# Kernel optimization log

Hardware: AMD Instinct MI355X
Metric: run time of the kernel (lower is better)

The kernel has to match this reference:

```python
import jax, jax.numpy as jnp
import numpy as np

DIM = 1024
NUM_HEADS = 16
DIM_HEAD = 64
POOL = 8  # int(sqrt(agent_num=64))
SCALE = DIM_HEAD ** -0.5


def setup_inputs() -> dict:
    key = jax.random.key(0)
    k1, k2, k3, k4 = jax.random.split(key, 4)
    inner = NUM_HEADS * DIM_HEAD
    x = jax.random.normal(k1, (4, 4096, DIM), dtype=jnp.float32)
    # qkv Linear (no bias): weight stored as (in, out) so forward is x @ Wqkv
    Wqkv = jax.random.normal(k2, (DIM, 3 * inner), dtype=jnp.float32) * (DIM ** -0.5)
    Wo = jax.random.normal(k3, (inner, DIM), dtype=jnp.float32) * (inner ** -0.5)
    bo = jax.random.normal(k4, (DIM,), dtype=jnp.float32) * 0.01
    return {"x": x, "Wqkv": Wqkv, "Wo": Wo, "bo": bo}


def reference(x, Wqkv, Wo, bo):
    b, t, _ = x.shape
    h, d = NUM_HEADS, DIM_HEAD
    qkv = x @ Wqkv                                   # [b, t, 3*h*d]
    qkv = qkv.reshape(b, t, 3, h, d)                 # split (qkv h d)
    qkv = jnp.transpose(qkv, (2, 0, 3, 1, 4))        # [3, b, h, t, d]
    q, k, v = qkv[0], qkv[1], qkv[2]
    # AdaptiveAvgPool2d((POOL, d)) on [b,h,t,d]: identity on d, mean-pool t -> POOL
    # (t divisible by POOL -> exact reshape+mean)
    agent = q.reshape(b, h, POOL, t // POOL, d).mean(axis=3)  # [b, h, P, d]
    # stage 1: agents attend over keys, aggregate values
    s1 = jnp.einsum('bhid,bhjd->bhij', agent * SCALE, k)      # [b, h, P, t]
    p1 = jax.nn.softmax(s1, axis=-1)
    v_agent = jnp.einsum('bhij,bhjd->bhid', p1, v)            # [b, h, P, d]
    # stage 2: queries attend over agent tokens
    s2 = jnp.einsum('bhid,bhjd->bhij', q * SCALE, agent)      # [b, h, t, P]
    p2 = jax.nn.softmax(s2, axis=-1)
    out = jnp.einsum('bhij,bhjd->bhid', p2, v_agent)          # [b, h, t, d]
    out = jnp.transpose(out, (0, 2, 1, 3)).reshape(b, t, h * d)
    return out @ Wo + bo
```

## Files before the change

### kernel.cpp

```cpp
#include <hip/hip_runtime.h>
#include <hip/hip_bf16.h>
#include <stdint.h>

typedef __bf16 bf16;
typedef __attribute__((ext_vector_type(8))) __bf16 bf16x8;
typedef __attribute__((ext_vector_type(4))) float f32x4;
typedef __attribute__((ext_vector_type(4))) unsigned int u32x4;

#define NH 16
#define DH 64
#define POOL 8
#define BATCH 4
#define SEQ 4096
#define DIMV 1024
#define QKV_N (3*DIMV)
#define M_TOTAL (BATCH*SEQ)
#define SCALE_F 0.125f
#define AGS_F (SCALE_F / 512.0f)
#define BH (BATCH*NH)
#define QKVSZ ((size_t)BH*SEQ*DH)
#define TCH 16
#define TCL (SEQ/TCH)
#define HP 128

#define AS1(p) ((const __attribute__((address_space(1))) void*)(p))
#define AS3(p) ((__attribute__((address_space(3))) void*)(p))
typedef const __attribute__((address_space(3))) char* lds_cp;

__global__ void prep(const float* __restrict__ x, bf16* __restrict__ xb,
                     const float* __restrict__ Wqkv, bf16* __restrict__ WqkvT,
                     const float* __restrict__ Wo, bf16* __restrict__ WoT) {
  __shared__ float tile[32][33];
  const int b = blockIdx.x;
  if (b < 8192) {
    size_t i = ((size_t)b * 256 + threadIdx.x) * 8;
    float4 f0 = *(const float4*)(x + i);
    float4 f1 = *(const float4*)(x + i + 4);
    bf16x8 o;
    o[0] = (bf16)f0.x; o[1] = (bf16)f0.y; o[2] = (bf16)f0.z; o[3] = (bf16)f0.w;
    o[4] = (bf16)f1.x; o[5] = (bf16)f1.y; o[6] = (bf16)f1.z; o[7] = (bf16)f1.w;
    *(bf16x8*)(xb + i) = o;
    return;
  }
  const float* in; bf16* out; int C, bx, by;
  if (b < 8192 + 3072) { int bb = b - 8192;  in = Wqkv; out = WqkvT; C = QKV_N; bx = bb % 96; by = bb / 96; }
  else                 { int bb = b - 11264; in = Wo;   out = WoT;   C = DIMV;  bx = bb % 32; by = bb / 32; }
  const int R = DIMV;
  int c0 = bx * 32, r0 = by * 32;
  int tx = threadIdx.x & 31, ty = threadIdx.x >> 5;
  for (int i = ty; i < 32; i += 8)
    tile[i][tx] = in[(size_t)(r0 + i) * C + c0 + tx];
  __syncthreads();
  for (int i = ty; i < 32; i += 8)
    out[(size_t)(c0 + i) * R + r0 + tx] = (bf16)tile[tx][i];
}

__global__ __launch_bounds__(512, 2)
void gemm1_qkv(const bf16* __restrict__ A, const bf16* __restrict__ B,
               bf16* __restrict__ qkvOut, float* __restrict__ agentSum) {
  constexpr int K1 = DIMV;
  constexpr int NI = K1 / 128;

  __shared__ __align__(16) bf16 LA[2][2][8192];
  __shared__ __align__(16) bf16 LB[2][2][8192];

  const int tid  = threadIdx.x;
  const int w    = tid >> 6;
  const int lane = tid & 63;
  const int wm = (w >> 2) * 128;
  const int wn = (w & 3) * 64;

  const int bid = blockIdx.x;
  const int swz = (bid & 7) * 96 + (bid >> 3);
  const int m0 = (swz / 12) * 256;
  const int n0 = (swz % 12) * 256;

  const int rT  = tid >> 3;
  const int csT = (((tid & 7) ^ (rT & 7)) << 3);
  const bf16* Ag = A + (size_t)(m0 + rT) * K1 + csT;
  const bf16* Bg = B + (size_t)(n0 + rT) * K1 + csT;

  const int rA = lane & 15, C = lane >> 4, xr = rA & 7;
  const unsigned s0 = (unsigned)(((0 * 4 + C) ^ xr) << 4);
  const unsigned s1 = (unsigned)(((1 * 4 + C) ^ xr) << 4);
  const unsigned aoff = (unsigned)((wm + rA) << 7);
  const unsigned boff = (unsigned)((wn + rA) << 7);

  f32x4 acc[8][4] = {};
  u32x4 aR[4][2], bR[4][2];

#define STG(arr, Gp, half, kofs) do {                                         \
    const bf16* _s = (Gp) + (size_t)((half) * 128) * K1 + (kofs);             \
    char* _d = (char*)&arr[half][0] + (w << 10);                              \
    __builtin_amdgcn_global_load_lds(AS1(_s), AS3(_d), 16, 0, 0);             \
    __builtin_amdgcn_global_load_lds(AS1(_s + 64 * K1), AS3(_d + 8192), 16, 0, 0); \
  } while (0)

#define DSR0(d, p)    asm volatile("ds_read_b128 %0, %1" : "=v"(d) : "v"(p))
#define DSR(d, p, o)  asm volatile("ds_read_b128 %0, %1 offset:" o : "=v"(d) : "v"(p))

#define READS_A(LAb, qm) do {                                                 \
    lds_cp _p0 = (lds_cp)(const char*)&LAb[0][0] + aoff + s0 + (qm) * 8192;   \
    lds_cp _p1 = (lds_cp)(const char*)&LAb[0][0] + aoff + s1 + (qm) * 8192;   \
    DSR0(aR[0][0], _p0); DSR(aR[1][0], _p0, "2048");                          \
    DSR(aR[2][0], _p0, "4096"); DSR(aR[3][0], _p0, "6144");                   \
    DSR0(aR[0][1], _p1); DSR(aR[1][1], _p1, "2048");                          \
    DSR(aR[2][1], _p1, "4096"); DSR(aR[3][1], _p1, "6144");                   \
  } while (0)

#define READS_B01(LBb) do {                                                   \
    lds_cp _p0 = (lds_cp)(const char*)&LBb[0][0] + boff + s0;                 \
    lds_cp _p1 = (lds_cp)(const char*)&LBb[0][0] + boff + s1;                 \
    DSR0(bR[0][0], _p0); DSR(bR[1][0], _p0, "2048");                          \
    DSR0(bR[0][1], _p1); DSR(bR[1][1], _p1, "2048");                          \
  } while (0)

#define READS_B23(LBb) do {                                                   \
    lds_cp _p0 = (lds_cp)(const char*)&LBb[0][0] + boff + s0;                 \
    lds_cp _p1 = (lds_cp)(const char*)&LBb[0][0] + boff + s1;                 \
    DSR(bR[2][0], _p0, "4096"); DSR(bR[3][0], _p0, "6144");                   \
    DSR(bR[2][1], _p1, "4096"); DSR(bR[3][1], _p1, "6144");                   \
  } while (0)

#define WAITL8 do { asm volatile("s_waitcnt lgkmcnt(8)");                     \
                    __builtin_amdgcn_sched_barrier(0); } while (0)

#define MFMA_Q(qm, qn) do {                                                   \
    asm volatile("s_waitcnt lgkmcnt(0)");                                     \
    __builtin_amdgcn_sched_barrier(0);                                        \
    __builtin_amdgcn_s_setprio(1);                                            \
    _Pragma("unroll")                                                         \
    for (int il = 0; il < 4; ++il)                                            \
      _Pragma("unroll")                                                       \
      for (int jj = 0; jj < 2; ++jj) {                                        \
        f32x4& ac = acc[(qm) * 4 + il][(qn) * 2 + jj];                        \
        ac = __builtin_amdgcn_mfma_f32_16x16x32_bf16(                         \
            __builtin_bit_cast(bf16x8, aR[il][0]),                            \
            __builtin_bit_cast(bf16x8, bR[(qn) * 2 + jj][0]), ac, 0, 0, 0);   \
        ac = __builtin_amdgcn_mfma_f32_16x16x32_bf16(                         \
            __builtin_bit_cast(bf16x8, aR[il][1]),                            \
            __builtin_bit_cast(bf16x8, bR[(qn) * 2 + jj][1]), ac, 0, 0, 0);   \
      }                                                                       \
    __builtin_amdgcn_s_setprio(0);                                            \
    __builtin_amdgcn_sched_barrier(0);                                        \
  } while (0)

#define BAR __builtin_amdgcn_s_barrier()

  STG(LA[0], Ag, 0, 0); STG(LA[0], Ag, 1, 0);
  STG(LB[0], Bg, 0, 0); STG(LB[0], Bg, 1, 0);
  STG(LB[1], Bg, 0, 64); STG(LB[1], Bg, 1, 64);
  asm volatile("s_waitcnt vmcnt(4)");
  __builtin_amdgcn_sched_barrier(0);
  BAR;

  int kk = 0;
  for (int i = 0; i < NI - 1; ++i, kk += 128) {
    READS_A(LA[0], 0); READS_B01(LB[0]);
    STG(LA[1], Ag, 0, kk + 64);
    WAITL8;
    BAR; MFMA_Q(0, 0); BAR;
    READS_B23(LB[0]);
    STG(LA[1], Ag, 1, kk + 64);
    BAR; MFMA_Q(0, 1); BAR;
    READS_A(LA[0], 1);
    STG(LB[0], Bg, 0, kk + 128);
    BAR; MFMA_Q(1, 0); BAR;
    STG(LB[0], Bg, 1, kk + 128);
    BAR; MFMA_Q(1, 1);
    asm volatile("s_waitcnt vmcnt(4)");
    __builtin_amdgcn_sched_barrier(0);
    BAR;
    READS_A(LA[1], 0); READS_B01(LB[1]);
    STG(LA[0], Ag, 0, kk + 128);
    WAITL8;
    BAR; MFMA_Q(0, 0); BAR;
    READS_B23(LB[1]);
    STG(LA[0], Ag, 1, kk + 128);
    BAR; MFMA_Q(0, 1); BAR;
    READS_A(LA[1], 1);
    STG(LB[1], Bg, 0, kk + 192);
    BAR; MFMA_Q(1, 0); BAR;
    STG(LB[1], Bg, 1, kk + 192);
    BAR; MFMA_Q(1, 1);
    asm volatile("s_waitcnt vmcnt(4)");
    __builtin_amdgcn_sched_barrier(0);
    BAR;
  }
  READS_A(LA[0], 0); READS_B01(LB[0]);
  STG(LA[1], Ag, 0, kk + 64);
  WAITL8;
  BAR; MFMA_Q(0, 0); BAR;
  READS_B23(LB[0]);
  STG(LA[1], Ag, 1, kk + 64);
  BAR; MFMA_Q(0, 1); BAR;
  READS_A(LA[0], 1);
  BAR; MFMA_Q(1, 0); BAR;
  MFMA_Q(1, 1);
  asm volatile("s_waitcnt vmcnt(0)");
  __builtin_amdgcn_sched_barrier(0);
  BAR;
  READS_A(LA[1], 0); READS_B01(LB[1]);
  WAITL8;
  BAR; MFMA_Q(0, 0); BAR;
  READS_B23(LB[1]);
  BAR; MFMA_Q(0, 1); BAR;
  READS_A(LA[1], 1);
  BAR; MFMA_Q(1, 0); BAR;
  MFMA_Q(1, 1);

#undef STG
#undef DSR0
#undef DSR
#undef READS_A
#undef READS_B01
#undef READS_B23
#undef WAITL8
#undef MFMA_Q
#undef BAR

  const int cr = (lane >> 4) * 4;
  const int cc = lane & 15;
  const int ncol  = n0 + wn;
  const int which = ncol >> 10;
  const int hh    = (ncol >> 6) & 15;
  const int rowb  = m0 + wm;
  const int bb_   = rowb >> 12;
  const int tb    = rowb & 4095;
  bf16* Cp = qkvOut + (size_t)which * QKVSZ + (size_t)(bb_ * NH + hh) * SEQ * DH;
#pragma unroll
  for (int i = 0; i < 8; ++i)
#pragma unroll
    for (int j = 0; j < 4; ++j)
#pragma unroll
      for (int r = 0; r < 4; ++r)
        Cp[(size_t)(tb + i * 16 + cr + r) * DH + j * 16 + cc] = (bf16)acc[i][j][r];

  if (which == 0) {
    const int pp = tb >> 9;
    float* ag = agentSum + ((size_t)(bb_ * NH + hh) * POOL + pp) * DH;
#pragma unroll
    for (int j = 0; j < 4; ++j) {
      float s = 0.f;
#pragma unroll
      for (int i = 0; i < 8; ++i)
        s += acc[i][j][0] + acc[i][j][1] + acc[i][j][2] + acc[i][j][3];
      s += __shfl_xor(s, 16);
      s += __shfl_xor(s, 32);
      if (lane < 16) atomicAdd(&ag[j * 16 + lane], s);
    }
  }
}

__global__ __launch_bounds__(512, 2)
void gemm2_256(const bf16* __restrict__ A, const bf16* __restrict__ B,
               float* __restrict__ Out, const float* __restrict__ bias) {
  constexpr int K2 = HP;

  __shared__ __align__(16) bf16 LA[2][2][8192];
  __shared__ __align__(16) bf16 LB[2][2][8192];

  const int tid  = threadIdx.x;
  const int w    = tid >> 6;
  const int lane = tid & 63;
  const int wm = (w >> 2) * 128;
  const int wn = (w & 3) * 64;

  const int bid = blockIdx.x;
  const int swz = (bid & 7) * 32 + (bid >> 3);
  const int m0 = (swz >> 2) * 256;
  const int n0 = (swz & 3) * 256;

  const int rT  = tid >> 3;
  const int csT = (((tid & 7) ^ (rT & 7)) << 3);
  const bf16* Ag = A + (size_t)(m0 + rT) * K2 + csT;
  const bf16* Bg = B + ((size_t)(m0 >> 12) * DIMV + n0 + rT) * K2 + csT;

  const int rA = lane & 15, C = lane >> 4, xr = rA & 7;
  const unsigned s0 = (unsigned)(((0 * 4 + C) ^ xr) << 4);
  const unsigned s1 = (unsigned)(((1 * 4 + C) ^ xr) << 4);
  const unsigned aoff = (unsigned)((wm + rA) << 7);
  const unsigned boff = (unsigned)((wn + rA) << 7);

  f32x4 acc[8][4] = {};
  u32x4 aR[4][2], bR[4][2];

#define STG(arr, Gp, half, kofs) do {                                         \
    const bf16* _s = (Gp) + (size_t)((half) * 128) * K2 + (kofs);             \
    char* _d = (char*)&arr[half][0] + (w << 10);                              \
    __builtin_amdgcn_global_load_lds(AS1(_s), AS3(_d), 16, 0, 0);             \
    __builtin_amdgcn_global_load_lds(AS1(_s + 64 * K2), AS3(_d + 8192), 16, 0, 0); \
  } while (0)

#define DSR0(d, p)    asm volatile("ds_read_b128 %0, %1" : "=v"(d) : "v"(p))
#define DSR(d, p, o)  asm volatile("ds_read_b128 %0, %1 offset:" o : "=v"(d) : "v"(p))

#define READS_A(LAb, qm) do {                                                 \
    lds_cp _p0 = (lds_cp)(const char*)&LAb[0][0] + aoff + s0 + (qm) * 8192;   \
    lds_cp _p1 = (lds_cp)(const char*)&LAb[0][0] + aoff + s1 + (qm) * 8192;   \
    DSR0(aR[0][0], _p0); DSR(aR[1][0], _p0, "2048");                          \
    DSR(aR[2][0], _p0, "4096"); DSR(aR[3][0], _p0, "6144");                   \
    DSR0(aR[0][1], _p1); DSR(aR[1][1], _p1, "2048");                          \
    DSR(aR[2][1], _p1, "4096"); DSR(aR[3][1], _p1, "6144");                   \
  } while (0)

#define READS_B01(LBb) do {                                                   \
    lds_cp _p0 = (lds_cp)(const char*)&LBb[0][0] + boff + s0;                 \
    lds_cp _p1 = (lds_cp)(const char*)&LBb[0][0] + boff + s1;                 \
    DSR0(bR[0][0], _p0); DSR(bR[1][0], _p0, "2048");                          \
    DSR0(bR[0][1], _p1); DSR(bR[1][1], _p1, "2048");                          \
  } while (0)

#define READS_B23(LBb) do {                                                   \
    lds_cp _p0 = (lds_cp)(const char*)&LBb[0][0] + boff + s0;                 \
    lds_cp _p1 = (lds_cp)(const char*)&LBb[0][0] + boff + s1;                 \
    DSR(bR[2][0], _p0, "4096"); DSR(bR[3][0], _p0, "6144");                   \
    DSR(bR[2][1], _p1, "4096"); DSR(bR[3][1], _p1, "6144");                   \
  } while (0)

#define WAITL8 do { asm volatile("s_waitcnt lgkmcnt(8)");                     \
                    __builtin_amdgcn_sched_barrier(0); } while (0)

#define MFMA_Q(qm, qn) do {                                                   \
    asm volatile("s_waitcnt lgkmcnt(0)");                                     \
    __builtin_amdgcn_sched_barrier(0);                                        \
    __builtin_amdgcn_s_setprio(1);                                            \
    _Pragma("unroll")                                                         \
    for (int il = 0; il < 4; ++il)                                            \
      _Pragma("unroll")                                                       \
      for (int jj = 0; jj < 2; ++jj) {                                        \
        f32x4& ac = acc[(qm) * 4 + il][(qn) * 2 + jj];                        \
        ac = __builtin_amdgcn_mfma_f32_16x16x32_bf16(                         \
            __builtin_bit_cast(bf16x8, aR[il][0]),                            \
            __builtin_bit_cast(bf16x8, bR[(qn) * 2 + jj][0]), ac, 0, 0, 0);   \
        ac = __builtin_amdgcn_mfma_f32_16x16x32_bf16(                         \
            __builtin_bit_cast(bf16x8, aR[il][1]),                            \
            __builtin_bit_cast(bf16x8, bR[(qn) * 2 + jj][1]), ac, 0, 0, 0);   \
      }                                                                       \
    __builtin_amdgcn_s_setprio(0);                                            \
    __builtin_amdgcn_sched_barrier(0);                                        \
  } while (0)

#define BAR __builtin_amdgcn_s_barrier()

  STG(LA[0], Ag, 0, 0); STG(LA[0], Ag, 1, 0);
  STG(LB[0], Bg, 0, 0); STG(LB[0], Bg, 1, 0);
  STG(LB[1], Bg, 0, 64); STG(LB[1], Bg, 1, 64);
  asm volatile("s_waitcnt vmcnt(4)");
  __builtin_amdgcn_sched_barrier(0);
  BAR;

  READS_A(LA[0], 0); READS_B01(LB[0]);
  STG(LA[1], Ag, 0, 64);
  WAITL8;
  BAR; MFMA_Q(0, 0); BAR;
  READS_B23(LB[0]);
  STG(LA[1], Ag, 1, 64);
  BAR; MFMA_Q(0, 1); BAR;
  READS_A(LA[0], 1);
  BAR; MFMA_Q(1, 0); BAR;
  MFMA_Q(1, 1);
  asm volatile("s_waitcnt vmcnt(0)");
  __builtin_amdgcn_sched_barrier(0);
  BAR;
  READS_A(LA[1], 0); READS_B01(LB[1]);
  WAITL8;
  BAR; MFMA_Q(0, 0); BAR;
  READS_B23(LB[1]);
  BAR; MFMA_Q(0, 1); BAR;
  READS_A(LA[1], 1);
  BAR; MFMA_Q(1, 0); BAR;
  MFMA_Q(1, 1);

#undef STG
#undef DSR0
#undef DSR
#undef READS_A
#undef READS_B01
#undef READS_B23
#undef WAITL8
#undef MFMA_Q
#undef BAR

  const int cr = (lane >> 4) * 4;
  const int cc = lane & 15;
  const int rowb = m0 + wm;
  float bb4[4];
#pragma unroll
  for (int j = 0; j < 4; ++j) bb4[j] = bias[n0 + wn + j * 16 + cc];
#pragma unroll
  for (int i = 0; i < 8; ++i)
#pragma unroll
    for (int j = 0; j < 4; ++j) {
      const int col = n0 + wn + j * 16 + cc;
#pragma unroll
      for (int r = 0; r < 4; ++r)
        Out[(size_t)(rowb + i * 16 + cr + r) * DIMV + col] = acc[i][j][r] + bb4[j];
    }
}

__global__ __launch_bounds__(256)
void attn_mid(const bf16* __restrict__ q, const bf16* __restrict__ k,
              const bf16* __restrict__ v, const float* __restrict__ agentSum,
              bf16* __restrict__ P2,
              float* __restrict__ pm, float* __restrict__ pl,
              float* __restrict__ pva) {
  const int tc = blockIdx.x, bh = blockIdx.y;
  const int tid = threadIdx.x;
  const int t0 = tc * TCL;

  __shared__ float agT[64][8];
  __shared__ float se[TCL][9];
  __shared__ float rm[4][8], rl[4][8];

  for (int i = tid; i < 512; i += 256) {
    int p = i >> 6, d = i & 63;
    agT[d][p] = agentSum[(size_t)bh * 512 + i] * AGS_F;
  }
  __syncthreads();

  const bf16* qrow = q + ((size_t)bh * SEQ + t0 + tid) * DH;
  const bf16* krow = k + ((size_t)bh * SEQ + t0 + tid) * DH;
  bf16x8 qv8[8], kv8[8];
#pragma unroll
  for (int dc = 0; dc < 8; ++dc) {
    qv8[dc] = *(const bf16x8*)(qrow + dc * 8);
    kv8[dc] = *(const bf16x8*)(krow + dc * 8);
  }
  float scq[8] = {}, sck[8] = {};
#pragma unroll
  for (int dc = 0; dc < 8; ++dc) {
#pragma unroll
    for (int e = 0; e < 8; ++e) {
      float qv = (float)qv8[dc][e];
      float kv = (float)kv8[dc][e];
      int d = dc * 8 + e;
      float4 a0 = *(const float4*)&agT[d][0];
      float4 a1 = *(const float4*)&agT[d][4];
      scq[0] += a0.x * qv; scq[1] += a0.y * qv; scq[2] += a0.z * qv; scq[3] += a0.w * qv;
      scq[4] += a1.x * qv; scq[5] += a1.y * qv; scq[6] += a1.z * qv; scq[7] += a1.w * qv;
      sck[0] += a0.x * kv; sck[1] += a0.y * kv; sck[2] += a0.z * kv; sck[3] += a0.w * kv;
      sck[4] += a1.x * kv; sck[5] += a1.y * kv; sck[6] += a1.z * kv; sck[7] += a1.w * kv;
    }
  }

  {
    float m = scq[0];
#pragma unroll
    for (int p = 1; p < 8; ++p) m = fmaxf(m, scq[p]);
    float wsum = 0.f, wgt[8];
#pragma unroll
    for (int p = 0; p < 8; ++p) { wgt[p] = __expf(scq[p] - m); wsum += wgt[p]; }
    float inv = 1.0f / wsum;
    int b = bh >> 4, h = bh & 15;
    bf16x8 o8;
#pragma unroll
    for (int p = 0; p < 8; ++p) o8[p] = (bf16)(wgt[p] * inv);
    *(bf16x8*)&P2[((size_t)(b * SEQ + t0 + tid)) * HP + h * 8] = o8;
  }

  float mx[8];
#pragma unroll
  for (int p = 0; p < 8; ++p) mx[p] = sck[p];
#pragma unroll
  for (int o = 32; o; o >>= 1)
#pragma unroll
    for (int p = 0; p < 8; ++p) mx[p] = fmaxf(mx[p], __shfl_xor(mx[p], o));
  if ((tid & 63) == 0)
#pragma unroll
    for (int p = 0; p < 8; ++p) rm[tid >> 6][p] = mx[p];
  __syncthreads();
  float m[8];
#pragma unroll
  for (int p = 0; p < 8; ++p)
    m[p] = fmaxf(fmaxf(rm[0][p], rm[1][p]), fmaxf(rm[2][p], rm[3][p]));

  float sl[8];
#pragma unroll
  for (int p = 0; p < 8; ++p) {
    float e = __expf(sck[p] - m[p]);
    se[tid][p] = e;
    sl[p] = e;
  }
#pragma unroll
  for (int o = 32; o; o >>= 1)
#pragma unroll
    for (int p = 0; p < 8; ++p) sl[p] += __shfl_xor(sl[p], o);
  if ((tid & 63) == 0)
#pragma unroll
    for (int p = 0; p < 8; ++p) rl[tid >> 6][p] = sl[p];
  __syncthreads();
  if (tid < 8) {
    float l = rl[0][tid] + rl[1][tid] + rl[2][tid] + rl[3][tid];
    pm[(size_t)(bh * TCH + tc) * 8 + tid] = m[tid];
    pl[(size_t)(bh * TCH + tc) * 8 + tid] = l;
  }
  __syncthreads();

  const int lane = tid & 63;
  const int wv = tid >> 6;
  const int dg = lane & 7;
  const int to = lane >> 3;
  const int p0 = wv * 2;
  const bf16* vb = v + ((size_t)bh * SEQ + t0 + to) * DH + dg * 8;
  float a0[8] = {}, a1[8] = {};
  for (int tl = to; tl < TCL; tl += 8) {
    bf16x8 v8 = *(const bf16x8*)(vb + (size_t)(tl - to) * DH);
    float w0 = se[tl][p0];
    float w1 = se[tl][p0 + 1];
#pragma unroll
    for (int e = 0; e < 8; ++e) {
      float vf = (float)v8[e];
      a0[e] += w0 * vf;
      a1[e] += w1 * vf;
    }
  }
#pragma unroll
  for (int o = 8; o <= 32; o <<= 1) {
#pragma unroll
    for (int e = 0; e < 8; ++e) {
      a0[e] += __shfl_xor(a0[e], o);
      a1[e] += __shfl_xor(a1[e], o);
    }
  }
  if (to == 0) {
    float* o0 = pva + ((size_t)(bh * TCH + tc) * 8 + p0) * DH + dg * 8;
    float* o1 = o0 + DH;
#pragma unroll
    for (int e = 0; e < 8; ++e) { o0[e] = a0[e]; o1[e] = a1[e]; }
  }
}

__global__ void combine_vag(const float* __restrict__ pm, const float* __restrict__ pl,
                            const float* __restrict__ pva, float* __restrict__ vag) {
  int bh = blockIdx.x;
#pragma unroll
  for (int e = threadIdx.x; e < 512; e += 256) {
    int p = e >> 6, d = e & 63;
    float M = -1e30f;
#pragma unroll
    for (int tc = 0; tc < TCH; ++tc)
      M = fmaxf(M, pm[(size_t)(bh * TCH + tc) * 8 + p]);
    float L = 0.f, acc = 0.f;
#pragma unroll
    for (int tc = 0; tc < TCH; ++tc) {
      float w = __expf(pm[(size_t)(bh * TCH + tc) * 8 + p] - M);
      L   += w * pl[(size_t)(bh * TCH + tc) * 8 + p];
      acc += w * pva[((size_t)(bh * TCH + tc) * 8 + p) * DH + d];
    }
    vag[(size_t)bh * 512 + e] = acc / L;
  }
}

__global__ void w2_build(const float* __restrict__ vag, const bf16* __restrict__ WoT,
                         bf16* __restrict__ W2T) {
  int b = blockIdx.y;
  int n = blockIdx.x * 16 + (threadIdx.x & 15);
  int h = threadIdx.x >> 4;
  __shared__ float vg[128][65];
  for (int i = threadIdx.x; i < 128 * 64; i += 256)
    vg[i >> 6][i & 63] = vag[(size_t)b * 128 * 64 + i];
  __syncthreads();
  float acc[8] = {};
  const bf16* wrow = WoT + (size_t)n * DIMV + h * 64;
#pragma unroll
  for (int dv = 0; dv < 8; ++dv) {
    bf16x8 wv = *(const bf16x8*)(wrow + dv * 8);
#pragma unroll
    for (int e = 0; e < 8; ++e) {
      float wf = (float)wv[e];
      int d = dv * 8 + e;
#pragma unroll
      for (int p = 0; p < 8; ++p) acc[p] += vg[h * 8 + p][d] * wf;
    }
  }
  bf16x8 o;
#pragma unroll
  for (int p = 0; p < 8; ++p) o[p] = (bf16)acc[p];
  *(bf16x8*)&W2T[((size_t)b * DIMV + n) * HP + h * 8] = o;
}

extern "C" void kernel_launch(void* const* d_in, const int* in_sizes, int n_in,
                              void* d_out, int out_size, void* d_ws, size_t ws_size,
                              hipStream_t stream) {
  const float* x    = (const float*)d_in[0];
  const float* Wqkv = (const float*)d_in[1];
  const float* Wo   = (const float*)d_in[2];
  const float* bo   = (const float*)d_in[3];
  float* out = (float*)d_out;

  char* ws = (char*)d_ws;
  bf16* WqkvT = (bf16*)ws;                                   ws += (size_t)QKV_N * DIMV * 2;
  bf16* WoT   = (bf16*)ws;                                   ws += (size_t)DIMV * DIMV * 2;
  bf16* qkv   = (bf16*)ws;                                   ws += 3 * QKVSZ * 2;
  char* wsu   = ws;                                          ws += (size_t)M_TOTAL * DIMV * 2;
  bf16*  xb    = (bf16*)wsu;
  bf16*  P2    = (bf16*)wsu;
  bf16*  W2T   = (bf16*)(wsu + (size_t)M_TOTAL * HP * 2);
  float* agent = (float*)ws;                                 ws += 512 * 64 * 4;
  float* pm    = (float*)ws;                                 ws += BH * TCH * 8 * 4;
  float* pl    = (float*)ws;                                 ws += BH * TCH * 8 * 4;
  float* pva   = (float*)ws;                                 ws += (size_t)BH * TCH * 8 * DH * 4;
  float* vag   = (float*)ws;                                 ws += 512 * 64 * 4;

  const bf16* qp = qkv;
  const bf16* kp = qkv + QKVSZ;
  const bf16* vp = qkv + 2 * QKVSZ;

  hipMemsetAsync(agent, 0, 512 * 64 * 4, stream);

  prep<<<12288, 256, 0, stream>>>(x, xb, Wqkv, WqkvT, Wo, WoT);

  gemm1_qkv<<<768, 512, 0, stream>>>(xb, WqkvT, qkv, agent);

  attn_mid<<<dim3(TCH, BH), 256, 0, stream>>>(qp, kp, vp, agent, P2, pm, pl, pva);

  combine_vag<<<BH, 256, 0, stream>>>(pm, pl, pva, vag);
  w2_build<<<dim3(DIMV / 16, BATCH), 256, 0, stream>>>(vag, WoT, W2T);

  gemm2_256<<<256, 512, 0, stream>>>(P2, W2T, out, bo);
}
```

Before: 295.3 us.

## Fold agent projection into weights; skip materializing Q and K

```diff
diff --git a/kernel.cpp b/kernel.cpp
--- a/kernel.cpp
+++ b/kernel.cpp
@@ -18,7 +18,6 @@
 #define SCALE_F 0.125f
 #define AGS_F (SCALE_F / 512.0f)
 #define BH (BATCH*NH)
-#define QKVSZ ((size_t)BH*SEQ*DH)
 #define TCH 16
 #define TCL (SEQ/TCH)
 #define HP 128
@@ -43,8 +42,8 @@
     return;
   }
   const float* in; bf16* out; int C, bx, by;
-  if (b < 8192 + 3072) { int bb = b - 8192;  in = Wqkv; out = WqkvT; C = QKV_N; bx = bb % 96; by = bb / 96; }
-  else                 { int bb = b - 11264; in = Wo;   out = WoT;   C = DIMV;  bx = bb % 32; by = bb / 32; }
+  if (b < 9216) { int bb = b - 8192; in = Wqkv; out = WqkvT; C = QKV_N; bx = 64 + (bb & 31); by = bb >> 5; }
+  else          { int bb = b - 9216; in = Wo;   out = WoT;   C = DIMV;  bx = bb & 31;        by = bb >> 5; }
   const int R = DIMV;
   int c0 = bx * 32, r0 = by * 32;
   int tx = threadIdx.x & 31, ty = threadIdx.x >> 5;
@@ -55,9 +54,75 @@
     out[(size_t)(c0 + i) * R + r0 + tx] = (bf16)tile[tx][i];
 }
 
+__global__ void pool_x(const bf16* __restrict__ xb, float* __restrict__ xpool) {
+  const int bid = blockIdx.x;
+  const int bucket = bid >> 3, slice = bid & 7;
+  const int b = bucket >> 3, p = bucket & 7;
+  const int tid = threadIdx.x;
+  const int co = tid & 127;
+  const int r0 = tid >> 7;
+  const bf16* src = xb + ((size_t)b * SEQ + p * 512 + slice * 64 + r0) * DIMV + co * 8;
+  float a[8] = {};
+  for (int r = 0; r < 64; r += 2) {
+    bf16x8 v = *(const bf16x8*)(src + (size_t)r * DIMV);
+#pragma unroll
+    for (int e = 0; e < 8; ++e) a[e] += (float)v[e];
+  }
+  float* dst = xpool + (size_t)bucket * DIMV + co * 8;
+#pragma unroll
+  for (int e = 0; e < 8; ++e) atomicAdd(&dst[e], a[e]);
+}
+
+__global__ void agent_build(const float* __restrict__ xpool, const float* __restrict__ Wqkv,
+                            float* __restrict__ agent_s) {
+  __shared__ float xp[256];
+  const int bid = blockIdx.x;
+  const int bp = bid >> 2, cs = bid & 3;
+  const int tid = threadIdx.x;
+  xp[tid] = xpool[(size_t)bp * DIMV + cs * 256 + tid];
+  __syncthreads();
+  float acc[4] = {};
+  const float* wbase = Wqkv + (size_t)(cs * 256) * QKV_N + tid * 4;
+#pragma unroll 8
+  for (int c = 0; c < 256; ++c) {
+    float xv = xp[c];
+    float4 wv = *(const float4*)(wbase + (size_t)c * QKV_N);
+    acc[0] += xv * wv.x; acc[1] += xv * wv.y; acc[2] += xv * wv.z; acc[3] += xv * wv.w;
+  }
+  float* dst = agent_s + (size_t)bp * DIMV + tid * 4;
+#pragma unroll
+  for (int j = 0; j < 4; ++j) atomicAdd(&dst[j], acc[j]);
+}
+
+__global__ void w2cat_build(const float* __restrict__ agent_s, const float* __restrict__ Wqkv,
+                            bf16* __restrict__ scw) {
+  __shared__ float ag[8][64];
+  const int bid = blockIdx.x;
+  const int ct = bid & 3, qk = (bid >> 2) & 1, h = (bid >> 3) & 15, b = bid >> 7;
+  const int tid = threadIdx.x;
+  for (int i = tid; i < 512; i += 256)
+    ag[i >> 6][i & 63] = agent_s[(size_t)(b * 8 + (i >> 6)) * DIMV + h * 64 + (i & 63)];
+  __syncthreads();
+  const int c = ct * 256 + tid;
+  const float* wrow = Wqkv + (size_t)c * QKV_N + qk * 1024 + h * 64;
+  float wv[64];
+#pragma unroll
+  for (int d4 = 0; d4 < 16; ++d4) {
+    float4 w4 = *(const float4*)(wrow + d4 * 4);
+    wv[d4 * 4] = w4.x; wv[d4 * 4 + 1] = w4.y; wv[d4 * 4 + 2] = w4.z; wv[d4 * 4 + 3] = w4.w;
+  }
+#pragma unroll
+  for (int p = 0; p < 8; ++p) {
+    float s = 0.f;
+#pragma unroll
+    for (int d = 0; d < 64; ++d) s += wv[d] * ag[p][d];
+    scw[((size_t)b * 256 + qk * 128 + h * 8 + p) * DIMV + c] = (bf16)(s * AGS_F);
+  }
+}
+
 __global__ __launch_bounds__(512, 2)
-void gemm1_qkv(const bf16* __restrict__ A, const bf16* __restrict__ B,
-               bf16* __restrict__ qkvOut, float* __restrict__ agentSum) {
+void vgemm(const bf16* __restrict__ A, const bf16* __restrict__ B,
+           bf16* __restrict__ vOut) {
   constexpr int K1 = DIMV;
   constexpr int NI = K1 / 128;
 
@@ -71,9 +136,9 @@
   const int wn = (w & 3) * 64;
 
   const int bid = blockIdx.x;
-  const int swz = (bid & 7) * 96 + (bid >> 3);
-  const int m0 = (swz / 12) * 256;
-  const int n0 = (swz % 12) * 256;
+  const int swz = (bid & 7) * 32 + (bid >> 3);
+  const int m0 = (swz >> 2) * 256;
+  const int n0 = (swz & 3) * 256;
 
   const int rT  = tid >> 3;
   const int csT = (((tid & 7) ^ (rT & 7)) << 3);
@@ -221,35 +286,250 @@
 
   const int cr = (lane >> 4) * 4;
   const int cc = lane & 15;
-  const int ncol  = n0 + wn;
-  const int which = ncol >> 10;
-  const int hh    = (ncol >> 6) & 15;
-  const int rowb  = m0 + wm;
-  const int bb_   = rowb >> 12;
-  const int tb    = rowb & 4095;
-  bf16* Cp = qkvOut + (size_t)which * QKVSZ + (size_t)(bb_ * NH + hh) * SEQ * DH;
+  const int ncol = n0 + wn;
+  const int hh   = ncol >> 6;
+  const int rowb = m0 + wm;
+  const int bb_  = rowb >> 12;
+  const int tb   = rowb & 4095;
+  bf16* Cp = vOut + (size_t)(bb_ * NH + hh) * SEQ * DH;
 #pragma unroll
   for (int i = 0; i < 8; ++i)
 #pragma unroll
     for (int j = 0; j < 4; ++j)
 #pragma unroll
       for (int r = 0; r < 4; ++r)
-        Cp[(size_t)(tb + i * 16 + cr + r) * DH + j * 16 + cc] = (bf16)acc[i][j][r];
-
-  if (which == 0) {
-    const int pp = tb >> 9;
-    float* ag = agentSum + ((size_t)(bb_ * NH + hh) * POOL + pp) * DH;
+        Cp[(size_t)(tb + i * 16 + cr + r) * DH + (ncol & 63) + j * 16 + cc] = (bf16)acc[i][j][r];
+}
+
+__global__ __launch_bounds__(256)
+void score_gemm(const bf16* __restrict__ A, const bf16* __restrict__ B,
+                float* __restrict__ SC) {
+  constexpr int K = DIMV;
+  __shared__ bf16 As[128 * 32];
+  __shared__ bf16 Bs[128 * 32];
+  const int tid  = threadIdx.x;
+  const int w    = tid >> 6;
+  const int lane = tid & 63;
+  const int m0 = blockIdx.y * 128, n0 = blockIdx.x * 128;
+  const int wm = (w & 1) * 64, wn = (w >> 1) * 64;
+
+  const bf16* Bb = B + (size_t)(m0 >> 12) * 256 * K;
+
+  f32x4 acc[4][4] = {};
+
+  const int g0  = w * 2;
+  const int rig = lane >> 2;
+  const int kcs = (lane & 3) ^ ((rig >> 1) & 3);
+  const bf16* Ap0 = A + (size_t)(m0 + g0 * 16 + rig) * K + kcs * 8;
+  const bf16* Ap1 = Ap0 + (size_t)16 * K;
+  const bf16* Bp0 = Bb + (size_t)(n0 + g0 * 16 + rig) * K + kcs * 8;
+  const bf16* Bp1 = Bp0 + (size_t)16 * K;
+  bf16* AsW0 = As + g0 * 512;
+  bf16* AsW1 = As + (g0 + 1) * 512;
+  bf16* BsW0 = Bs + g0 * 512;
+  bf16* BsW1 = Bs + (g0 + 1) * 512;
+
+  for (int k0 = 0; k0 < K; k0 += 32) {
+    __syncthreads();
+    __builtin_amdgcn_global_load_lds(AS1(Ap0 + k0), AS3(AsW0), 16, 0, 0);
+    __builtin_amdgcn_global_load_lds(AS1(Ap1 + k0), AS3(AsW1), 16, 0, 0);
+    __builtin_amdgcn_global_load_lds(AS1(Bp0 + k0), AS3(BsW0), 16, 0, 0);
+    __builtin_amdgcn_global_load_lds(AS1(Bp1 + k0), AS3(BsW1), 16, 0, 0);
+    __syncthreads();
+
+    bf16x8 a[4], b[4];
+    const int C = lane >> 4;
+#pragma unroll
+    for (int i = 0; i < 4; ++i) {
+      int ar = wm + i * 16 + (lane & 15);
+      int sw = C ^ ((ar >> 1) & 3);
+      a[i] = *(const bf16x8*)&As[ar * 32 + sw * 8];
+    }
 #pragma unroll
     for (int j = 0; j < 4; ++j) {
-      float s = 0.f;
-#pragma unroll
-      for (int i = 0; i < 8; ++i)
-        s += acc[i][j][0] + acc[i][j][1] + acc[i][j][2] + acc[i][j][3];
-      s += __shfl_xor(s, 16);
-      s += __shfl_xor(s, 32);
-      if (lane < 16) atomicAdd(&ag[j * 16 + lane], s);
+      int br = wn + j * 16 + (lane & 15);
+      int sw = C ^ ((br >> 1) & 3);
+      b[j] = *(const bf16x8*)&Bs[br * 32 + sw * 8];
     }
-  }
+#pragma unroll
+    for (int i = 0; i < 4; ++i)
+#pragma unroll
+      for (int j = 0; j < 4; ++j)
+        acc[i][j] = __builtin_amdgcn_mfma_f32_16x16x32_bf16(a[i], b[j], acc[i][j], 0, 0, 0);
+  }
+
+  const int cr = (lane >> 4) * 4;
+  const int cc = lane & 15;
+#pragma unroll
+  for (int i = 0; i < 4; ++i) {
+#pragma unroll
+    for (int j = 0; j < 4; ++j) {
+      int col = n0 + wn + j * 16 + cc;
+      int qk = col >> 7, h = (col >> 3) & 15, p = col & 7;
+#pragma unroll
+      for (int r = 0; r < 4; ++r) {
+        int row = m0 + wm + i * 16 + cr + r;
+        int b = row >> 12, t = row & 4095;
+        SC[((size_t)(b * NH + h) * SEQ + t) * 16 + qk * 8 + p] = acc[i][j][r];
+      }
+    }
+  }
+}
+
+__global__ __launch_bounds__(256)
+void attn_mid(const float* __restrict__ SC, const bf16* __restrict__ v,
+              bf16* __restrict__ P2,
+              float* __restrict__ pm, float* __restrict__ pl,
+              float* __restrict__ pva) {
+  const int tc = blockIdx.x, bh = blockIdx.y;
+  const int tid = threadIdx.x;
+  const int t0 = tc * TCL;
+
+  __shared__ float se[TCL][9];
+  __shared__ float rm[4][8], rl[4][8];
+
+  const float* scp = SC + ((size_t)bh * SEQ + t0 + tid) * 16;
+  float4 sq0 = *(const float4*)(scp);
+  float4 sq1 = *(const float4*)(scp + 4);
+  float4 sk0 = *(const float4*)(scp + 8);
+  float4 sk1 = *(const float4*)(scp + 12);
+  float scq[8] = {sq0.x, sq0.y, sq0.z, sq0.w, sq1.x, sq1.y, sq1.z, sq1.w};
+  float sck[8] = {sk0.x, sk0.y, sk0.z, sk0.w, sk1.x, sk1.y, sk1.z, sk1.w};
+
+  {
+    float m = scq[0];
+#pragma unroll
+    for (int p = 1; p < 8; ++p) m = fmaxf(m, scq[p]);
+    float wsum = 0.f, wgt[8];
+#pragma unroll
+    for (int p = 0; p < 8; ++p) { wgt[p] = __expf(scq[p] - m); wsum += wgt[p]; }
+    float inv = 1.0f / wsum;
+    int b = bh >> 4, h = bh & 15;
+    bf16x8 o8;
+#pragma unroll
+    for (int p = 0; p < 8; ++p) o8[p] = (bf16)(wgt[p] * inv);
+    *(bf16x8*)&P2[((size_t)(b * SEQ + t0 + tid)) * HP + h * 8] = o8;
+  }
+
+  float mx[8];
+#pragma unroll
+  for (int p = 0; p < 8; ++p) mx[p] = sck[p];
+#pragma unroll
+  for (int o = 32; o; o >>= 1)
+#pragma unroll
+    for (int p = 0; p < 8; ++p) mx[p] = fmaxf(mx[p], __shfl_xor(mx[p], o));
+  if ((tid & 63) == 0)
+#pragma unroll
+    for (int p = 0; p < 8; ++p) rm[tid >> 6][p] = mx[p];
+  __syncthreads();
+  float m[8];
+#pragma unroll
+  for (int p = 0; p < 8; ++p)
+    m[p] = fmaxf(fmaxf(rm[0][p], rm[1][p]), fmaxf(rm[2][p], rm[3][p]));
+
+  float sl[8];
+#pragma unroll
+  for (int p = 0; p < 8; ++p) {
+    float e = __expf(sck[p] - m[p]);
+    se[tid][p] = e;
+    sl[p] = e;
+  }
+#pragma unroll
+  for (int o = 32; o; o >>= 1)
+#pragma unroll
+    for (int p = 0; p < 8; ++p) sl[p] += __shfl_xor(sl[p], o);
+  if ((tid & 63) == 0)
+#pragma unroll
+    for (int p = 0; p < 8; ++p) rl[tid >> 6][p] = sl[p];
+  __syncthreads();
+  if (tid < 8) {
+    float l = rl[0][tid] + rl[1][tid] + rl[2][tid] + rl[3][tid];
+    pm[(size_t)(bh * TCH + tc) * 8 + tid] = m[tid];
+    pl[(size_t)(bh * TCH + tc) * 8 + tid] = l;
+  }
+  __syncthreads();
+
+  const int lane = tid & 63;
+  const int wv = tid >> 6;
+  const int dg = lane & 7;
+  const int to = lane >> 3;
+  const int p0 = wv * 2;
+  const bf16* vb = v + ((size_t)bh * SEQ + t0 + to) * DH + dg * 8;
+  float a0[8] = {}, a1[8] = {};
+  for (int tl = to; tl < TCL; tl += 8) {
+    bf16x8 v8 = *(const bf16x8*)(vb + (size_t)(tl - to) * DH);
+    float w0 = se[tl][p0];
+    float w1 = se[tl][p0 + 1];
+#pragma unroll
+    for (int e = 0; e < 8; ++e) {
+      float vf = (float)v8[e];
+      a0[e] += w0 * vf;
+      a1[e] += w1 * vf;
+    }
+  }
+#pragma unroll
+  for (int o = 8; o <= 32; o <<= 1) {
+#pragma unroll
+    for (int e = 0; e < 8; ++e) {
+      a0[e] += __shfl_xor(a0[e], o);
+      a1[e] += __shfl_xor(a1[e], o);
+    }
+  }
+  if (to == 0) {
+    float* o0 = pva + ((size_t)(bh * TCH + tc) * 8 + p0) * DH + dg * 8;
+    float* o1 = o0 + DH;
+#pragma unroll
+    for (int e = 0; e < 8; ++e) { o0[e] = a0[e]; o1[e] = a1[e]; }
+  }
+}
+
+__global__ void combine_vag(const float* __restrict__ pm, const float* __restrict__ pl,
+                            const float* __restrict__ pva, float* __restrict__ vag) {
+  int bh = blockIdx.x;
+#pragma unroll
+  for (int e = threadIdx.x; e < 512; e += 256) {
+    int p = e >> 6, d = e & 63;
+    float M = -1e30f;
+#pragma unroll
+    for (int tc = 0; tc < TCH; ++tc)
+      M = fmaxf(M, pm[(size_t)(bh * TCH + tc) * 8 + p]);
+    float L = 0.f, acc = 0.f;
+#pragma unroll
+    for (int tc = 0; tc < TCH; ++tc) {
+      float w = __expf(pm[(size_t)(bh * TCH + tc) * 8 + p] - M);
+      L   += w * pl[(size_t)(bh * TCH + tc) * 8 + p];
+      acc += w * pva[((size_t)(bh * TCH + tc) * 8 + p) * DH + d];
+    }
+    vag[(size_t)bh * 512 + e] = acc / L;
+  }
+}
+
+__global__ void w2_build(const float* __restrict__ vag, const bf16* __restrict__ WoT,
+                         bf16* __restrict__ W2T) {
+  int b = blockIdx.y;
+  int n = blockIdx.x * 16 + (threadIdx.x & 15);
+  int h = threadIdx.x >> 4;
+  __shared__ float vg[128][65];
+  for (int i = threadIdx.x; i < 128 * 64; i += 256)
+    vg[i >> 6][i & 63] = vag[(size_t)b * 128 * 64 + i];
+  __syncthreads();
+  float acc[8] = {};
+  const bf16* wrow = WoT + (size_t)n * DIMV + h * 64;
+#pragma unroll
+  for (int dv = 0; dv < 8; ++dv) {
+    bf16x8 wv = *(const bf16x8*)(wrow + dv * 8);
+#pragma unroll
+    for (int e = 0; e < 8; ++e) {
+      float wf = (float)wv[e];
+      int d = dv * 8 + e;
+#pragma unroll
+      for (int p = 0; p < 8; ++p) acc[p] += vg[h * 8 + p][d] * wf;
+    }
+  }
+  bf16x8 o;
+#pragma unroll
+  for (int p = 0; p < 8; ++p) o[p] = (bf16)acc[p];
+  *(bf16x8*)&W2T[((size_t)b * DIMV + n) * HP + h * 8] = o;
 }
 
 __global__ __launch_bounds__(512, 2)
@@ -399,187 +679,6 @@
     }
 }
 
-__global__ __launch_bounds__(256)
-void attn_mid(const bf16* __restrict__ q, const bf16* __restrict__ k,
-              const bf16* __restrict__ v, const float* __restrict__ agentSum,
-              bf16* __restrict__ P2,
-              float* __restrict__ pm, float* __restrict__ pl,
-              float* __restrict__ pva) {
-  const int tc = blockIdx.x, bh = blockIdx.y;
-  const int tid = threadIdx.x;
-  const int t0 = tc * TCL;
-
-  __shared__ float agT[64][8];
-  __shared__ float se[TCL][9];
-  __shared__ float rm[4][8], rl[4][8];
-
-  for (int i = tid; i < 512; i += 256) {
-    int p = i >> 6, d = i & 63;
-    agT[d][p] = agentSum[(size_t)bh * 512 + i] * AGS_F;
-  }
-  __syncthreads();
-
-  const bf16* qrow = q + ((size_t)bh * SEQ + t0 + tid) * DH;
-  const bf16* krow = k + ((size_t)bh * SEQ + t0 + tid) * DH;
-  bf16x8 qv8[8], kv8[8];
-#pragma unroll
-  for (int dc = 0; dc < 8; ++dc) {
-    qv8[dc] = *(const bf16x8*)(qrow + dc * 8);
-    kv8[dc] = *(const bf16x8*)(krow + dc * 8);
-  }
-  float scq[8] = {}, sck[8] = {};
-#pragma unroll
-  for (int dc = 0; dc < 8; ++dc) {
-#pragma unroll
-    for (int e = 0; e < 8; ++e) {
-      float qv = (float)qv8[dc][e];
-      float kv = (float)kv8[dc][e];
-      int d = dc * 8 + e;
-      float4 a0 = *(const float4*)&agT[d][0];
-      float4 a1 = *(const float4*)&agT[d][4];
-      scq[0] += a0.x * qv; scq[1] += a0.y * qv; scq[2] += a0.z * qv; scq[3] += a0.w * qv;
-      scq[4] += a1.x * qv; scq[5] += a1.y * qv; scq[6] += a1.z * qv; scq[7] += a1.w * qv;
-      sck[0] += a0.x * kv; sck[1] += a0.y * kv; sck[2] += a0.z * kv; sck[3] += a0.w * kv;
-      sck[4] += a1.x * kv; sck[5] += a1.y * kv; sck[6] += a1.z * kv; sck[7] += a1.w * kv;
-    }
-  }
-
-  {
-    float m = scq[0];
-#pragma unroll
-    for (int p = 1; p < 8; ++p) m = fmaxf(m, scq[p]);
-    float wsum = 0.f, wgt[8];
-#pragma unroll
-    for (int p = 0; p < 8; ++p) { wgt[p] = __expf(scq[p] - m); wsum += wgt[p]; }
-    float inv = 1.0f / wsum;
-    int b = bh >> 4, h = bh & 15;
-    bf16x8 o8;
-#pragma unroll
-    for (int p = 0; p < 8; ++p) o8[p] = (bf16)(wgt[p] * inv);
-    *(bf16x8*)&P2[((size_t)(b * SEQ + t0 + tid)) * HP + h * 8] = o8;
-  }
-
-  float mx[8];
-#pragma unroll
-  for (int p = 0; p < 8; ++p) mx[p] = sck[p];
-#pragma unroll
-  for (int o = 32; o; o >>= 1)
-#pragma unroll
-    for (int p = 0; p < 8; ++p) mx[p] = fmaxf(mx[p], __shfl_xor(mx[p], o));
-  if ((tid & 63) == 0)
-#pragma unroll
-    for (int p = 0; p < 8; ++p) rm[tid >> 6][p] = mx[p];
-  __syncthreads();
-  float m[8];
-#pragma unroll
-  for (int p = 0; p < 8; ++p)
-    m[p] = fmaxf(fmaxf(rm[0][p], rm[1][p]), fmaxf(rm[2][p], rm[3][p]));
-
-  float sl[8];
-#pragma unroll
-  for (int p = 0; p < 8; ++p) {
-    float e = __expf(sck[p] - m[p]);
-    se[tid][p] = e;
-    sl[p] = e;
-  }
-#pragma unroll
-  for (int o = 32; o; o >>= 1)
-#pragma unroll
-    for (int p = 0; p < 8; ++p) sl[p] += __shfl_xor(sl[p], o);
-  if ((tid & 63) == 0)
-#pragma unroll
-    for (int p = 0; p < 8; ++p) rl[tid >> 6][p] = sl[p];
-  __syncthreads();
-  if (tid < 8) {
-    float l = rl[0][tid] + rl[1][tid] + rl[2][tid] + rl[3][tid];
-    pm[(size_t)(bh * TCH + tc) * 8 + tid] = m[tid];
-    pl[(size_t)(bh * TCH + tc) * 8 + tid] = l;
-  }
-  __syncthreads();
-
-  const int lane = tid & 63;
-  const int wv = tid >> 6;
-  const int dg = lane & 7;
-  const int to = lane >> 3;
-  const int p0 = wv * 2;
-  const bf16* vb = v + ((size_t)bh * SEQ + t0 + to) * DH + dg * 8;
-  float a0[8] = {}, a1[8] = {};
-  for (int tl = to; tl < TCL; tl += 8) {
-    bf16x8 v8 = *(const bf16x8*)(vb + (size_t)(tl - to) * DH);
-    float w0 = se[tl][p0];
-    float w1 = se[tl][p0 + 1];
-#pragma unroll
-    for (int e = 0; e < 8; ++e) {
-      float vf = (float)v8[e];
-      a0[e] += w0 * vf;
-      a1[e] += w1 * vf;
-    }
-  }
-#pragma unroll
-  for (int o = 8; o <= 32; o <<= 1) {
-#pragma unroll
-    for (int e = 0; e < 8; ++e) {
-      a0[e] += __shfl_xor(a0[e], o);
-      a1[e] += __shfl_xor(a1[e], o);
-    }
-  }
-  if (to == 0) {
-    float* o0 = pva + ((size_t)(bh * TCH + tc) * 8 + p0) * DH + dg * 8;
-    float* o1 = o0 + DH;
-#pragma unroll
-    for (int e = 0; e < 8; ++e) { o0[e] = a0[e]; o1[e] = a1[e]; }
-  }
-}
-
-__global__ void combine_vag(const float* __restrict__ pm, const float* __restrict__ pl,
-                            const float* __restrict__ pva, float* __restrict__ vag) {
-  int bh = blockIdx.x;
-#pragma unroll
-  for (int e = threadIdx.x; e < 512; e += 256) {
-    int p = e >> 6, d = e & 63;
-    float M = -1e30f;
-#pragma unroll
-    for (int tc = 0; tc < TCH; ++tc)
-      M = fmaxf(M, pm[(size_t)(bh * TCH + tc) * 8 + p]);
-    float L = 0.f, acc = 0.f;
-#pragma unroll
-    for (int tc = 0; tc < TCH; ++tc) {
-      float w = __expf(pm[(size_t)(bh * TCH + tc) * 8 + p] - M);
-      L   += w * pl[(size_t)(bh * TCH + tc) * 8 + p];
-      acc += w * pva[((size_t)(bh * TCH + tc) * 8 + p) * DH + d];
-    }
-    vag[(size_t)bh * 512 + e] = acc / L;
-  }
-}
-
-__global__ void w2_build(const float* __restrict__ vag, const bf16* __restrict__ WoT,
-                         bf16* __restrict__ W2T) {
-  int b = blockIdx.y;
-  int n = blockIdx.x * 16 + (threadIdx.x & 15);
-  int h = threadIdx.x >> 4;
-  __shared__ float vg[128][65];
-  for (int i = threadIdx.x; i < 128 * 64; i += 256)
-    vg[i >> 6][i & 63] = vag[(size_t)b * 128 * 64 + i];
-  __syncthreads();
-  float acc[8] = {};
-  const bf16* wrow = WoT + (size_t)n * DIMV + h * 64;
-#pragma unroll
-  for (int dv = 0; dv < 8; ++dv) {
-    bf16x8 wv = *(const bf16x8*)(wrow + dv * 8);
-#pragma unroll
-    for (int e = 0; e < 8; ++e) {
-      float wf = (float)wv[e];
-      int d = dv * 8 + e;
-#pragma unroll
-      for (int p = 0; p < 8; ++p) acc[p] += vg[h * 8 + p][d] * wf;
-    }
-  }
-  bf16x8 o;
-#pragma unroll
-  for (int p = 0; p < 8; ++p) o[p] = (bf16)acc[p];
-  *(bf16x8*)&W2T[((size_t)b * DIMV + n) * HP + h * 8] = o;
-}
-
 extern "C" void kernel_launch(void* const* d_in, const int* in_sizes, int n_in,
                               void* d_out, int out_size, void* d_ws, size_t ws_size,
                               hipStream_t stream) {
@@ -590,30 +689,36 @@
   float* out = (float*)d_out;
 
   char* ws = (char*)d_ws;
-  bf16* WqkvT = (bf16*)ws;                                   ws += (size_t)QKV_N * DIMV * 2;
-  bf16* WoT   = (bf16*)ws;                                   ws += (size_t)DIMV * DIMV * 2;
-  bf16* qkv   = (bf16*)ws;                                   ws += 3 * QKVSZ * 2;
-  char* wsu   = ws;                                          ws += (size_t)M_TOTAL * DIMV * 2;
-  bf16*  xb    = (bf16*)wsu;
-  bf16*  P2    = (bf16*)wsu;
-  bf16*  W2T   = (bf16*)(wsu + (size_t)M_TOTAL * HP * 2);
-  float* agent = (float*)ws;                                 ws += 512 * 64 * 4;
-  float* pm    = (float*)ws;                                 ws += BH * TCH * 8 * 4;
-  float* pl    = (float*)ws;                                 ws += BH * TCH * 8 * 4;
-  float* pva   = (float*)ws;                                 ws += (size_t)BH * TCH * 8 * DH * 4;
-  float* vag   = (float*)ws;                                 ws += 512 * 64 * 4;
-
-  const bf16* qp = qkv;
-  const bf16* kp = qkv + QKVSZ;
-  const bf16* vp = qkv + 2 * QKVSZ;
-
-  hipMemsetAsync(agent, 0, 512 * 64 * 4, stream);
-
-  prep<<<12288, 256, 0, stream>>>(x, xb, Wqkv, WqkvT, Wo, WoT);
-
-  gemm1_qkv<<<768, 512, 0, stream>>>(xb, WqkvT, qkv, agent);
-
-  attn_mid<<<dim3(TCH, BH), 256, 0, stream>>>(qp, kp, vp, agent, P2, pm, pl, pva);
+  bf16*  WqkvT  = (bf16*)ws;                                 ws += (size_t)QKV_N * DIMV * 2;
+  bf16*  WoT    = (bf16*)ws;                                 ws += (size_t)DIMV * DIMV * 2;
+  bf16*  vpl    = (bf16*)ws;                                 ws += (size_t)BH * SEQ * DH * 2;
+  char*  wsu    = ws;                                        ws += (size_t)M_TOTAL * DIMV * 2;
+  bf16*  xb     = (bf16*)wsu;
+  bf16*  P2     = (bf16*)wsu;
+  bf16*  W2T    = (bf16*)(wsu + (size_t)M_TOTAL * HP * 2);
+  float* SC     = (float*)ws;                                ws += (size_t)BH * SEQ * 16 * 4;
+  bf16*  scw    = (bf16*)ws;                                 ws += (size_t)BATCH * 256 * DIMV * 2;
+  float* xpool  = (float*)ws;                                ws += 32 * DIMV * 4;
+  float* agent_s= (float*)ws;                                ws += 32 * DIMV * 4;
+  float* pm     = (float*)ws;                                ws += BH * TCH * 8 * 4;
+  float* pl     = (float*)ws;                                ws += BH * TCH * 8 * 4;
+  float* pva    = (float*)ws;                                ws += (size_t)BH * TCH * 8 * DH * 4;
+  float* vag    = (float*)ws;                                ws += 512 * 64 * 4;
+
+  hipMemsetAsync(xpool, 0, 32 * DIMV * 4, stream);
+  hipMemsetAsync(agent_s, 0, 32 * DIMV * 4, stream);
+
+  prep<<<10240, 256, 0, stream>>>(x, xb, Wqkv, WqkvT, Wo, WoT);
+
+  pool_x<<<256, 256, 0, stream>>>(xb, xpool);
+  agent_build<<<128, 256, 0, stream>>>(xpool, Wqkv, agent_s);
+  w2cat_build<<<512, 256, 0, stream>>>(agent_s, Wqkv, scw);
+
+  vgemm<<<256, 512, 0, stream>>>(xb, WqkvT + (size_t)2048 * DIMV, vpl);
+
+  score_gemm<<<dim3(2, 128), 256, 0, stream>>>(xb, scw, SC);
+
+  attn_mid<<<dim3(TCH, BH), 256, 0, stream>>>(SC, vpl, P2, pm, pl, pva);
 
   combine_vag<<<BH, 256, 0, stream>>>(pm, pl, pva, vag);
   w2_build<<<dim3(DIMV / 16, BATCH), 256, 0, stream>>>(vag, WoT, W2T);
```

New measurement: 306.9 us. 1.04x slower.
